# Performance work log

Hardware: AMD Instinct MI355X
Metric: run time of the kernel (lower is better)

The kernel has to match this reference:

```python
import jax, jax.numpy as jnp
import numpy as np
import math

B, N, C_IN, C_OUT, K, M, DIM = 8, 8192, 64, 128, 16, 16, 3


def setup_inputs() -> dict:
    key = jax.random.key(0)
    ks = jax.random.split(key, 12)
    features = jax.random.normal(ks[0], (B, N, C_IN), dtype=jnp.float32)
    input_pts = jax.random.uniform(ks[1], (B, N, DIM), dtype=jnp.float32)
    output_pts = jax.random.uniform(ks[2], (B, N, DIM), dtype=jnp.float32)
    indices = jax.random.randint(ks[3], (B, N, K), 0, N)
    # main conv weight [C_in, M, C_out], uniform(-bound, bound) as in torch init
    bound = math.sqrt(3.0) * math.sqrt(2.0 / (C_IN + C_OUT))
    weight = jax.random.uniform(ks[4], (C_IN, M, C_OUT), minval=-bound, maxval=bound, dtype=jnp.float32)
    bias = jnp.zeros((C_OUT,), dtype=jnp.float32)
    # kernel element centers inside unit ball [dim, M]
    centers = jax.random.uniform(ks[5], (DIM, M), minval=-1.0, maxval=1.0, dtype=jnp.float32) * 0.57
    # MLP: l1 (dim*M -> 2M), l2 (2M -> M), l3 (M -> M); torch Linear layout [out, in]
    def lin(k, fan_in, fan_out):
        lim = 1.0 / math.sqrt(fan_in)
        kw, kb = jax.random.split(k)
        w = jax.random.uniform(kw, (fan_out, fan_in), minval=-lim, maxval=lim, dtype=jnp.float32)
        b = jax.random.uniform(kb, (fan_out,), minval=-lim, maxval=lim, dtype=jnp.float32)
        return w, b
    l1_w, l1_b = lin(ks[6], DIM * M, 2 * M)
    l2_w, l2_b = lin(ks[7], 2 * M, M)
    l3_w, l3_b = lin(ks[8], M, M)
    return {"features": features, "input_pts": input_pts, "output_pts": output_pts,
            "indices": indices, "centers": centers, "weight": weight, "bias": bias,
            "l1_w": l1_w, "l1_b": l1_b, "l2_w": l2_w, "l2_b": l2_b, "l3_w": l3_w, "l3_b": l3_b}


def _gather(x, idx):
    # x: [B, N, D], idx: [B, No, K] -> [B, No, K, D]
    b, no, k = idx.shape
    flat = jnp.take_along_axis(x, idx.reshape(b, no * k, 1), axis=1)
    return flat.reshape(b, no, k, x.shape[-1])


def reference(features, input_pts, output_pts, indices, centers, weight, bias,
              l1_w, l1_b, l2_w, l2_b, l3_w, l3_b):
    # Gather neighbor features and points
    feats_nb = _gather(features, indices)            # [B, No, K, C_in]
    pts = _gather(input_pts, indices)                # [B, No, K, dim]
    pts = pts - output_pts[:, :, None, :]            # relative coords
    # distances to kernel centers: [B, No, K, dim, M] -> [B, No, K, dim*M]
    d = pts[..., :, None] - centers                  # centers [dim, M]
    d = d.reshape(d.shape[0], d.shape[1], d.shape[2], -1)
    # 3-layer MLP with relu
    d = jax.nn.relu(d @ l1_w.T + l1_b)
    d = jax.nn.relu(d @ l2_w.T + l2_b)
    d = jax.nn.relu(d @ l3_w.T + l3_b)               # [B, No, K, M]
    # weighted neighbor aggregation: contract over K neighbors
    agg = jnp.einsum('bnkc,bnkm->bncm', feats_nb, d)  # [B, No, C_in, M]
    bsz, no = agg.shape[0], agg.shape[1]
    agg = agg.reshape(bsz, no, -1)                    # [B, No, C_in*M]
    out = agg @ weight.reshape(-1, weight.shape[-1])  # [B, No, C_out]
    out = out / feats_nb.shape[2]                     # divide by K
    out = out + bias
    return (out, output_pts)
```

## Files before the change

kernel.cpp:

```cpp
#include <hip/hip_runtime.h>

#define BATCH 8
#define NPTS  8192
#define CIN   64
#define COUT  128
#define KNN   16
#define MD    16
#define PTS   16
#define PTSC  32
#define DT_STR 264
#define AGG_STRIDE 1032

#define NWT    (COUT * CIN * MD)
#define NFBF   (BATCH * NPTS * CIN)
#define NPTS_G (BATCH * NPTS)

typedef __attribute__((ext_vector_type(8))) short short8;
typedef __attribute__((ext_vector_type(4))) short short4v;
typedef __attribute__((ext_vector_type(4))) float f32x4;
typedef __attribute__((ext_vector_type(2))) float f32x2;

__device__ __forceinline__ short f2bf(float f) {
  unsigned u = __float_as_uint(f);
  u = (u + 0x7fffu + ((u >> 16) & 1u)) >> 16;
  return (short)u;
}

__global__ __launch_bounds__(256) void prep_kernel(
    const float* __restrict__ weight, const float* __restrict__ opts,
    const float* __restrict__ feats, const float* __restrict__ centers,
    const float* __restrict__ l1_w, const float* __restrict__ l1_b,
    const float* __restrict__ l2_w, const float* __restrict__ l3_w,
    short* __restrict__ Wt, short* __restrict__ fbf,
    short* __restrict__ l2bf, short* __restrict__ l3bf, float* __restrict__ Gc4,
    float* __restrict__ out_tail, int mode) {
  int tid = blockIdx.x * 256 + threadIdx.x;
  if (mode >= 1 && tid < NWT) {
    int co, o;
    if (mode == 3) {
      int j = tid & 7, quad = (tid >> 3) & 3, lrow = (tid >> 5) & 15;
      int kb = (tid >> 9) & 31, wv = tid >> 14;
      co = wv * 16 + lrow;
      o = kb * 32 + quad * 8 + j;
    } else {
      co = tid >> 10;
      o = tid & 1023;
    }
    int k;
    if (mode == 3) {
      int r = o & 3, q = (o >> 2) & 3, m = (o >> 4) & 15, ct = o >> 8;
      k = ct * 256 + q * 64 + r * 16 + m;
    } else {
      k = o;
    }
    Wt[tid] = f2bf(weight[(size_t)k * COUT + co]);
  }
  if (mode >= 2 && tid < NFBF / 4) {
    int row = tid >> 4, lr = tid & 15;
    const float* fr = feats + ((size_t)row << 6) + lr;
    short4v v = {f2bf(fr[0]), f2bf(fr[16]), f2bf(fr[32]), f2bf(fr[48])};
    *(short4v*)(fbf + ((size_t)row << 6) + lr * 4) = v;
  }
  if (mode == 3) {
    if (tid < 512) l2bf[tid] = f2bf(l2_w[tid]);
    if (tid < 256) l3bf[tid] = f2bf(l3_w[tid]);
    if (tid < 32) {
      float g0 = 0.f, g1 = 0.f, g2 = 0.f, cc = l1_b[tid];
      const float* wr = l1_w + tid * 48;
#pragma unroll
      for (int m = 0; m < 16; ++m) { g0 += wr[m]; g1 += wr[16 + m]; g2 += wr[32 + m]; }
#pragma unroll
      for (int i = 0; i < 48; ++i) cc -= wr[i] * centers[i];
      Gc4[tid * 4 + 0] = g0; Gc4[tid * 4 + 1] = g1; Gc4[tid * 4 + 2] = g2; Gc4[tid * 4 + 3] = cc;
    }
  }
  if (tid < BATCH * NPTS * 3) out_tail[tid] = opts[tid];
}

__global__ __launch_bounds__(512, 4) void conv_kernel(
    const int* __restrict__ indices, const short* __restrict__ fbf,
    const short* __restrict__ Wt, const short* __restrict__ l2bf,
    const short* __restrict__ l3bf, const float* __restrict__ Gc4,
    const float* __restrict__ l2_b, const float* __restrict__ l3_b,
    const float* __restrict__ input_pts, const float* __restrict__ output_pts,
    const float* __restrict__ bias, float* __restrict__ out) {
  __shared__ __align__(16) short s_agg[PTSC * AGG_STRIDE];

  const int t = threadIdx.x, blk = blockIdx.x;
  const int w = ((blk & 7) << 8) | (blk >> 3);
  const int batch = w >> 8, n0 = (w & 255) * PTSC;
  const int lane = t & 63, wv = t >> 6, quad = lane >> 4, lrow = lane & 15;
  const size_t bbase = (size_t)batch * NPTS;

  const int myid = indices[(bbase + n0) * KNN + t];
  const float* op = output_pts + (bbase + n0 + wv * 4 + quad) * 3;
  const float* ip = input_pts + (bbase + myid) * 3;
  const float px = ip[0] - op[0], py = ip[1] - op[1], pz = ip[2] - op[2];

  f32x4 G[8];
#pragma unroll
  for (int j = 0; j < 8; ++j) G[j] = *(const f32x4*)(Gc4 + (quad * 8 + j) * 4);
  const short8  w2f = *(const short8*)(l2bf + lrow * 32 + quad * 8);
  const short4v w3f = *(const short4v*)(l3bf + lrow * 16 + quad * 4);
  const f32x4 b2f = *(const f32x4*)(l2_b + quad * 4);
  const float b3v = l3_b[lrow];
  const f32x4 b3f = {b3v, b3v, b3v, b3v};

  short4v g[4][4];
#pragma unroll
  for (int pp = 0; pp < 4; ++pp)
#pragma unroll
    for (int j = 0; j < 4; ++j) {
      const int idn = __shfl(myid, pp * 16 + quad * 4 + j);
      g[pp][j] = *(const short4v*)(fbf + ((bbase + idn) << 6) + lrow * 4);
    }

  short8 h1f[4];
#pragma unroll
  for (int pp = 0; pp < 4; ++pp) {
    const float qx = __shfl(px, pp * 16 + lrow);
    const float qy = __shfl(py, pp * 16 + lrow);
    const float qz = __shfl(pz, pp * 16 + lrow);
#pragma unroll
    for (int j = 0; j < 8; ++j) {
      const f32x4 Gx = G[j];
      h1f[pp][j] = f2bf(fmaxf(fmaf(Gx[0], qx, fmaf(Gx[1], qy, fmaf(Gx[2], qz, Gx[3]))), 0.f));
    }
  }

  f32x4 h2[4];
#pragma unroll
  for (int pp = 0; pp < 4; ++pp)
    h2[pp] = __builtin_amdgcn_mfma_f32_16x16x32_bf16(w2f, h1f[pp], b2f, 0, 0, 0);
  short4v h2f[4];
#pragma unroll
  for (int pp = 0; pp < 4; ++pp)
#pragma unroll
    for (int r = 0; r < 4; ++r) h2f[pp][r] = f2bf(fmaxf(h2[pp][r], 0.f));

  f32x4 h3[4];
#pragma unroll
  for (int pp = 0; pp < 4; ++pp)
    h3[pp] = __builtin_amdgcn_mfma_f32_16x16x16bf16_1k(h2f[pp], w3f, b3f, 0, 0, 0);
  short4v dfr[4];
#pragma unroll
  for (int pp = 0; pp < 4; ++pp)
#pragma unroll
    for (int r = 0; r < 4; ++r) dfr[pp][r] = f2bf(fmaxf(h3[pp][r], 0.f) * 0.0625f);

#pragma unroll
  for (int pp = 0; pp < 4; ++pp) {
    const int pt = wv * 4 + pp;
    const short4v g0 = g[pp][0], g1 = g[pp][1], g2 = g[pp][2], g3 = g[pp][3];
#pragma unroll
    for (int ct = 0; ct < 4; ++ct) {
      const short4v afr = {g0[ct], g1[ct], g2[ct], g3[ct]};
      const f32x4 dd = __builtin_amdgcn_mfma_f32_16x16x16bf16_1k(
          afr, dfr[pp], (f32x4){0.f, 0.f, 0.f, 0.f}, 0, 0, 0);
      short4v sv;
#pragma unroll
      for (int r = 0; r < 4; ++r) sv[r] = f2bf(dd[r]);
      *(short4v*)&s_agg[pt * AGG_STRIDE + ct * 256 + lrow * 16 + quad * 4] = sv;
    }
  }

  const int co = wv * 16 + lrow;
  const short* wp = Wt + wv * 16384 + lrow * 32 + quad * 8;
  short8 Bpf[4];
#pragma unroll
  for (int i = 0; i < 4; ++i) Bpf[i] = *(const short8*)(wp + i * 512);

  asm volatile("s_waitcnt lgkmcnt(0)" ::: "memory");
  __builtin_amdgcn_s_barrier();
  asm volatile("" ::: "memory");

  f32x4 acc0 = {0.f, 0.f, 0.f, 0.f};
  f32x4 acc1 = {0.f, 0.f, 0.f, 0.f};
  const short* a0 = s_agg + lrow * AGG_STRIDE + quad * 8;
  const short* a1 = a0 + 16 * AGG_STRIDE;
  __builtin_amdgcn_s_setprio(1);
#pragma unroll
  for (int kb = 0; kb < 32; ++kb) {
    const short8 bfr = Bpf[kb & 3];
    if (kb < 28) Bpf[kb & 3] = *(const short8*)(wp + (kb + 4) * 512);
    const short8 av0 = *(const short8*)(a0 + kb * 32);
    const short8 av1 = *(const short8*)(a1 + kb * 32);
    acc0 = __builtin_amdgcn_mfma_f32_16x16x32_bf16(av0, bfr, acc0, 0, 0, 0);
    acc1 = __builtin_amdgcn_mfma_f32_16x16x32_bf16(av1, bfr, acc1, 0, 0, 0);
  }
  __builtin_amdgcn_s_setprio(0);
  const float bi = bias[co];
#pragma unroll
  for (int r = 0; r < 4; ++r) {
    const int p0 = quad * 4 + r;
    out[(bbase + n0 + p0) * COUT + co] = acc0[r] + bi;
    out[(bbase + n0 + 16 + p0) * COUT + co] = acc1[r] + bi;
  }
}

template <int MODE>
__global__ __launch_bounds__(256, 3) void ptconv_mono(
    const float* __restrict__ features, const float* __restrict__ input_pts,
    const float* __restrict__ output_pts, const int* __restrict__ indices,
    const float* __restrict__ centers, const float* __restrict__ weight,
    const float* __restrict__ bias,
    const float* __restrict__ l1_w, const float* __restrict__ l1_b,
    const float* __restrict__ l2_w, const float* __restrict__ l2_b,
    const float* __restrict__ l3_w, const float* __restrict__ l3_b,
    const short* __restrict__ Wt, const short* __restrict__ fbf,
    float* __restrict__ out) {
  __shared__ __align__(16) short s_dT[MD * DT_STR];
  __shared__ __align__(16) short s_agg[PTS * AGG_STRIDE];
  __shared__ __align__(16) int   s_idx[PTS * KNN];

  const int t = threadIdx.x;
  const int blk = blockIdx.x;
  const int batch = blk >> 9;
  const int n0 = (blk & 511) * PTS;
  const int lane = t & 63;
  const int wv = t >> 6;
  const int quad = lane >> 4;
  const int lrow = lane & 15;

  s_idx[t] = indices[((size_t)batch * NPTS + n0) * KNN + t];
  {
    const int pt = t >> 4;
    const int id = s_idx[t];
    const float* op = &output_pts[((size_t)batch * NPTS + n0 + pt) * 3];
    const float* ip = &input_pts[((size_t)batch * NPTS + id) * 3];
    const float px = ip[0] - op[0], py = ip[1] - op[1], pz = ip[2] - op[2];
    f32x2 dv[24];
    {
      const f32x2 px2 = {px, px}, py2 = {py, py}, pz2 = {pz, pz};
      const f32x2* cx = (const f32x2*)centers;
      const f32x2* cy = (const f32x2*)(centers + 16);
      const f32x2* cz = (const f32x2*)(centers + 32);
#pragma unroll
      for (int i = 0; i < 8; ++i) {
        dv[i] = px2 - cx[i]; dv[8 + i] = py2 - cy[i]; dv[16 + i] = pz2 - cz[i];
      }
    }
    float h1[32];
#pragma unroll
    for (int o = 0; o < 32; ++o) {
      const f32x2* wr = (const f32x2*)(l1_w + o * 48);
      f32x2 acc = {0.f, 0.f};
#pragma unroll
      for (int i = 0; i < 24; ++i) acc += dv[i] * wr[i];
      h1[o] = fmaxf(acc[0] + acc[1] + l1_b[o], 0.f);
    }
    f32x2 h1v[16];
#pragma unroll
    for (int i = 0; i < 16; ++i) h1v[i] = (f32x2){h1[2 * i], h1[2 * i + 1]};
    float h2[16];
#pragma unroll
    for (int o = 0; o < 16; ++o) {
      const f32x2* wr = (const f32x2*)(l2_w + o * 32);
      f32x2 acc = {0.f, 0.f};
#pragma unroll
      for (int i = 0; i < 16; ++i) acc += h1v[i] * wr[i];
      h2[o] = fmaxf(acc[0] + acc[1] + l2_b[o], 0.f);
    }
    f32x2 h2v[8];
#pragma unroll
    for (int i = 0; i < 8; ++i) h2v[i] = (f32x2){h2[2 * i], h2[2 * i + 1]};
#pragma unroll
    for (int o = 0; o < 16; ++o) {
      const f32x2* wr = (const f32x2*)(l3_w + o * 16);
      f32x2 acc = {0.f, 0.f};
#pragma unroll
      for (int i = 0; i < 8; ++i) acc += h2v[i] * wr[i];
      s_dT[o * DT_STR + t] = f2bf(fmaxf(acc[0] + acc[1] + l3_b[o], 0.f));
    }
  }
  __syncthreads();
  {
#pragma unroll
    for (int pp = 0; pp < 4; ++pp) {
      const int pt = wv * 4 + pp;
      const short4v bfrag = *(const short4v*)&s_dT[lrow * DT_STR + pt * 16 + quad * 4];
      const int4 idx4 = *(const int4*)&s_idx[pt * 16 + quad * 4];
#pragma unroll
      for (int ct = 0; ct < 4; ++ct) {
        short4v afr;
#pragma unroll
        for (int j = 0; j < 4; ++j) {
          const int id = ((const int*)&idx4)[j];
          const size_t base = ((size_t)batch * NPTS + id) * CIN;
          if (MODE >= 2) afr[j] = fbf[base + lrow * 4 + ct];
          else           afr[j] = f2bf(features[base + ct * 16 + lrow]);
        }
        f32x4 dd = __builtin_amdgcn_mfma_f32_16x16x16bf16_1k(
            afr, bfrag, (f32x4){0.f, 0.f, 0.f, 0.f}, 0, 0, 0);
#pragma unroll
        for (int r = 0; r < 4; ++r) {
          const int rr = (r + quad) & 3;
          const int c = ct * 16 + quad * 4 + rr;
          s_agg[pt * AGG_STRIDE + c * 16 + lrow] = f2bf(dd[rr]);
        }
      }
    }
  }
  __syncthreads();
  {
    f32x4 acc0 = {0.f, 0.f, 0.f, 0.f};
    f32x4 acc1 = {0.f, 0.f, 0.f, 0.f};
    const int co0 = wv * 32 + lrow;
    const int co1 = co0 + 16;
    const short* arow = s_agg + lrow * AGG_STRIDE + quad * 8;
#pragma unroll 4
    for (int kb = 0; kb < 32; ++kb) {
      const short8 a = *(const short8*)(arow + kb * 32);
      short8 b0, b1;
      if (MODE >= 1) {
        b0 = *(const short8*)(Wt + (size_t)co0 * 1024 + kb * 32 + quad * 8);
        b1 = *(const short8*)(Wt + (size_t)co1 * 1024 + kb * 32 + quad * 8);
      } else {
#pragma unroll
        for (int j = 0; j < 8; ++j) {
          const int kk = kb * 32 + quad * 8 + j;
          b0[j] = f2bf(weight[(size_t)kk * COUT + co0]);
          b1[j] = f2bf(weight[(size_t)kk * COUT + co1]);
        }
      }
      acc0 = __builtin_amdgcn_mfma_f32_16x16x32_bf16(a, b0, acc0, 0, 0, 0);
      acc1 = __builtin_amdgcn_mfma_f32_16x16x32_bf16(a, b1, acc1, 0, 0, 0);
    }
    const float bi0 = bias[co0], bi1 = bias[co1];
#pragma unroll
    for (int r = 0; r < 4; ++r) {
      const int pt = quad * 4 + r;
      const size_t rowo = ((size_t)batch * NPTS + n0 + pt) * COUT;
      out[rowo + co0] = acc0[r] * 0.0625f + bi0;
      out[rowo + co1] = acc1[r] * 0.0625f + bi1;
    }
  }
}

extern "C" void kernel_launch(void* const* d_in, const int* in_sizes, int n_in,
                              void* d_out, int out_size, void* d_ws, size_t ws_size,
                              hipStream_t stream) {
  const float* features   = (const float*)d_in[0];
  const float* input_pts  = (const float*)d_in[1];
  const float* output_pts = (const float*)d_in[2];
  const int*   indices    = (const int*)d_in[3];
  const float* centers    = (const float*)d_in[4];
  const float* weight     = (const float*)d_in[5];
  const float* bias       = (const float*)d_in[6];
  const float* l1_w       = (const float*)d_in[7];
  const float* l1_b       = (const float*)d_in[8];
  const float* l2_w       = (const float*)d_in[9];
  const float* l2_b       = (const float*)d_in[10];
  const float* l3_w       = (const float*)d_in[11];
  const float* l3_b       = (const float*)d_in[12];
  float* out = (float*)d_out;

  short* Wt   = (short*)d_ws;
  short* fbf  = Wt + NWT;
  short* l2bf = fbf + NFBF;
  short* l3bf = l2bf + 512;
  float* Gc4  = (float*)(l3bf + 256);
  const size_t need3 = (size_t)(NWT + NFBF + 512 + 256) * 2 + 512;

  int mode = 0;
  if (ws_size >= need3) mode = 3;
  else if (ws_size >= (size_t)(NWT + NFBF) * 2) mode = 2;
  else if (ws_size >= (size_t)NWT * 2) mode = 1;

  float* out_tail = out + (size_t)BATCH * NPTS * COUT;
  const int prep_elems = (mode >= 2) ? (NFBF / 4) : BATCH * NPTS * 3;
  prep_kernel<<<(prep_elems + 255) / 256, 256, 0, stream>>>(
      weight, output_pts, features, centers, l1_w, l1_b, l2_w, l3_w,
      Wt, fbf, l2bf, l3bf, Gc4, out_tail, mode);

  if (mode == 3) {
    conv_kernel<<<NPTS_G / PTSC, 512, 0, stream>>>(
        indices, fbf, Wt, l2bf, l3bf, Gc4, l2_b, l3_b, input_pts, output_pts, bias, out);
  } else if (mode == 2) {
    ptconv_mono<2><<<NPTS_G / PTS, 256, 0, stream>>>(features, input_pts, output_pts, indices,
        centers, weight, bias, l1_w, l1_b, l2_w, l2_b, l3_w, l3_b, Wt, fbf, out);
  } else if (mode == 1) {
    ptconv_mono<1><<<NPTS_G / PTS, 256, 0, stream>>>(features, input_pts, output_pts, indices,
        centers, weight, bias, l1_w, l1_b, l2_w, l2_b, l3_w, l3_b, Wt, fbf, out);
  } else {
    ptconv_mono<0><<<NPTS_G / PTS, 256, 0, stream>>>(features, input_pts, output_pts, indices,
        centers, weight, bias, l1_w, l1_b, l2_w, l2_b, l3_w, l3_b, Wt, fbf, out);
  }
}
```

Measured before the change: 144.5 us.

## Switch final GEMM to 32x32x16 MFMA with split-K across waves and LDS reduction

```diff
diff --git a/kernel.cpp b/kernel.cpp
--- a/kernel.cpp
+++ b/kernel.cpp
@@ -17,6 +17,7 @@
 
 typedef __attribute__((ext_vector_type(8))) short short8;
 typedef __attribute__((ext_vector_type(4))) short short4v;
+typedef __attribute__((ext_vector_type(16))) float f32x16;
 typedef __attribute__((ext_vector_type(4))) float f32x4;
 typedef __attribute__((ext_vector_type(2))) float f32x2;
 
@@ -36,22 +37,22 @@
     float* __restrict__ out_tail, int mode) {
   int tid = blockIdx.x * 256 + threadIdx.x;
   if (mode >= 1 && tid < NWT) {
-    int co, o;
+    int co, s;
     if (mode == 3) {
-      int j = tid & 7, quad = (tid >> 3) & 3, lrow = (tid >> 5) & 15;
-      int kb = (tid >> 9) & 31, wv = tid >> 14;
-      co = wv * 16 + lrow;
-      o = kb * 32 + quad * 8 + j;
+      int e = tid & 7, c = (tid >> 3) & 31, sh = (tid >> 8) & 1;
+      int ks = (tid >> 9) & 63, tc = tid >> 15;
+      co = tc * 32 + c;
+      s = ks * 16 + sh * 8 + e;
     } else {
       co = tid >> 10;
-      o = tid & 1023;
+      s = tid & 1023;
     }
     int k;
     if (mode == 3) {
-      int r = o & 3, q = (o >> 2) & 3, m = (o >> 4) & 15, ct = o >> 8;
+      int r = s & 3, q = (s >> 2) & 3, m = (s >> 4) & 15, ct = s >> 8;
       k = ct * 256 + q * 64 + r * 16 + m;
     } else {
-      k = o;
+      k = s;
     }
     Wt[tid] = f2bf(weight[(size_t)k * COUT + co]);
   }
@@ -164,8 +165,10 @@
     }
   }
 
-  const int co = wv * 16 + lrow;
-  const short* wp = Wt + wv * 16384 + lrow * 32 + quad * 8;
+  const int kh = wv >> 2, tc = wv & 3;
+  const int col = lane & 31, sh = lane >> 5;
+  const short* wp = Wt + ((tc * 64 + kh * 32) * 64 + sh * 32 + col) * 8;
+  const short* ap = s_agg + col * AGG_STRIDE + kh * 512 + sh * 8;
   short8 Bpf[4];
 #pragma unroll
   for (int i = 0; i < 4; ++i) Bpf[i] = *(const short8*)(wp + i * 512);
@@ -174,27 +177,43 @@
   __builtin_amdgcn_s_barrier();
   asm volatile("" ::: "memory");
 
-  f32x4 acc0 = {0.f, 0.f, 0.f, 0.f};
-  f32x4 acc1 = {0.f, 0.f, 0.f, 0.f};
-  const short* a0 = s_agg + lrow * AGG_STRIDE + quad * 8;
-  const short* a1 = a0 + 16 * AGG_STRIDE;
+  f32x16 acc;
+#pragma unroll
+  for (int i = 0; i < 16; ++i) acc[i] = 0.f;
   __builtin_amdgcn_s_setprio(1);
 #pragma unroll
-  for (int kb = 0; kb < 32; ++kb) {
-    const short8 bfr = Bpf[kb & 3];
-    if (kb < 28) Bpf[kb & 3] = *(const short8*)(wp + (kb + 4) * 512);
-    const short8 av0 = *(const short8*)(a0 + kb * 32);
-    const short8 av1 = *(const short8*)(a1 + kb * 32);
-    acc0 = __builtin_amdgcn_mfma_f32_16x16x32_bf16(av0, bfr, acc0, 0, 0, 0);
-    acc1 = __builtin_amdgcn_mfma_f32_16x16x32_bf16(av1, bfr, acc1, 0, 0, 0);
+  for (int ks = 0; ks < 32; ++ks) {
+    const short8 bfr = Bpf[ks & 3];
+    if (ks < 28) Bpf[ks & 3] = *(const short8*)(wp + (ks + 4) * 512);
+    const short8 av = *(const short8*)(ap + ks * 16);
+    acc = __builtin_amdgcn_mfma_f32_32x32x16_bf16(av, bfr, acc, 0, 0, 0);
   }
   __builtin_amdgcn_s_setprio(0);
-  const float bi = bias[co];
-#pragma unroll
-  for (int r = 0; r < 4; ++r) {
-    const int p0 = quad * 4 + r;
-    out[(bbase + n0 + p0) * COUT + co] = acc0[r] + bi;
-    out[(bbase + n0 + 16 + p0) * COUT + co] = acc1[r] + bi;
+
+  __builtin_amdgcn_s_barrier();
+  asm volatile("" ::: "memory");
+  float* ps = (float*)s_agg;
+  if (kh == 1) {
+#pragma unroll
+    for (int r4 = 0; r4 < 4; ++r4) {
+      const f32x4 v = {acc[r4 * 4], acc[r4 * 4 + 1], acc[r4 * 4 + 2], acc[r4 * 4 + 3]};
+      *(f32x4*)(ps + tc * 1280 + lane * 20 + r4 * 4) = v;
+    }
+  }
+  asm volatile("s_waitcnt lgkmcnt(0)" ::: "memory");
+  __builtin_amdgcn_s_barrier();
+  asm volatile("" ::: "memory");
+  if (kh == 0) {
+    const float bi = bias[tc * 32 + col];
+    f32x4 pr[4];
+#pragma unroll
+    for (int r4 = 0; r4 < 4; ++r4)
+      pr[r4] = *(const f32x4*)(ps + tc * 1280 + lane * 20 + r4 * 4);
+#pragma unroll
+    for (int reg = 0; reg < 16; ++reg) {
+      const int row = (reg & 3) + 8 * (reg >> 2) + 4 * sh;
+      out[(bbase + n0 + row) * COUT + tc * 32 + col] = acc[reg] + pr[reg >> 2][reg & 3] + bi;
+    }
   }
 }
 
```

After: 135.9 us. 5.9% less time.
